# Optimization experiments

Measured on AMD Instinct MI355X. Metric: run time of the kernel, lower is better.

Reference implementation:

```python
import jax, jax.numpy as jnp
import numpy as np

N = 50000
NUM_GRAPHS = 64
EPS = 1e-16  # PyG softmax denominator epsilon


def _gat_conv(x, src, dst, W, a_src, a_dst, b, heads, out_ch):
    n = x.shape[0]
    h = (x @ W).reshape(n, heads, out_ch)                    # [N,H,C]
    al_s = jnp.einsum('nhc,hc->nh', h, a_src)                # [N,H]
    al_d = jnp.einsum('nhc,hc->nh', h, a_dst)                # [N,H]
    e = jax.nn.leaky_relu(al_s[src] + al_d[dst], 0.2)        # [E,H]
    emax = jax.ops.segment_max(e, dst, num_segments=n)       # [N,H]
    ee = jnp.exp(e - emax[dst])
    den = jax.ops.segment_sum(ee, dst, num_segments=n)       # [N,H]
    alpha = ee / (den[dst] + EPS)                            # [E,H]
    msg = h[src] * alpha[:, :, None]                         # [E,H,C]
    out = jax.ops.segment_sum(msg, dst, num_segments=n)      # [N,H,C]
    return out.reshape(n, heads * out_ch) + b


def setup_inputs() -> dict:
    key = jax.random.key(0)
    ks = jax.random.split(key, 16)
    E = 250000
    x = jax.random.normal(ks[0], (N, 11), dtype=jnp.float32)
    edge_index = jax.random.randint(ks[1], (2, E), 0, N, dtype=jnp.int64)
    batch = jnp.sort(jax.random.randint(ks[2], (N,), 0, NUM_GRAPHS, dtype=jnp.int64))
    def glorot(k, shape):
        fan = shape[0] + shape[-1]
        return jax.random.uniform(k, shape, jnp.float32, -1.0, 1.0) * np.sqrt(6.0 / fan)
    return {
        'x': x, 'edge_index': edge_index, 'batch': batch,
        'W1': glorot(ks[3], (11, 8 * 128)),
        'a1s': glorot(ks[4], (8, 128)), 'a1d': glorot(ks[5], (8, 128)),
        'b1': jnp.zeros((8 * 128,), jnp.float32),
        'W2': glorot(ks[6], (1024, 8 * 64)),
        'a2s': glorot(ks[7], (8, 64)), 'a2d': glorot(ks[8], (8, 64)),
        'b2': jnp.zeros((8 * 64,), jnp.float32),
        'W3': glorot(ks[9], (512, 4 * 32)),
        'a3s': glorot(ks[10], (4, 32)), 'a3d': glorot(ks[11], (4, 32)),
        'b3': jnp.zeros((4 * 32,), jnp.float32),
        'Wout': glorot(ks[12], (128, 1)),
        'bout': jnp.zeros((1,), jnp.float32),
    }


def reference(x, edge_index, batch, W1, a1s, a1d, b1, W2, a2s, a2d, b2,
              W3, a3s, a3d, b3, Wout, bout):
    n = x.shape[0]
    # GATConv adds self-loops by default
    loop = jnp.arange(n, dtype=edge_index.dtype)
    src = jnp.concatenate([edge_index[0], loop])
    dst = jnp.concatenate([edge_index[1], loop])
    h = jax.nn.leaky_relu(_gat_conv(x, src, dst, W1, a1s, a1d, b1, 8, 128), 0.01)
    h = jax.nn.leaky_relu(_gat_conv(h, src, dst, W2, a2s, a2d, b2, 8, 64), 0.01)
    h = jax.nn.leaky_relu(_gat_conv(h, src, dst, W3, a3s, a3d, b3, 4, 32), 0.01)
    # global mean pool over graphs
    sums = jax.ops.segment_sum(h, batch, num_segments=NUM_GRAPHS)      # [G,128]
    cnt = jax.ops.segment_sum(jnp.ones((n,), h.dtype), batch, num_segments=NUM_GRAPHS)
    pooled = sums / jnp.maximum(cnt, 1.0)[:, None]
    return pooled @ Wout + bout                                        # [G,1]
```

## Files before the change

### kernel.cpp

```cpp
#include <hip/hip_runtime.h>

#define EPS 1e-16f

typedef __attribute__((ext_vector_type(8))) short short8;
typedef __attribute__((ext_vector_type(4))) float f32x4;

__device__ __forceinline__ float b2f(unsigned short u) {
    return __uint_as_float(((unsigned)u) << 16);
}
__device__ __forceinline__ unsigned short f2b(float f) {
    unsigned u = __float_as_uint(f);
    u += 0x7fffu + ((u >> 16) & 1u);
    return (unsigned short)(u >> 16);
}

typedef __attribute__((address_space(3))) void lds_vp;
typedef __attribute__((address_space(1))) const void glb_vp;
__device__ __forceinline__ void load_lds16(const unsigned short* g,
                                           unsigned short* l) {
    __builtin_amdgcn_global_load_lds((glb_vp*)g, (lds_vp*)l, 16, 0, 0);
}

__global__ void init_deg_kernel(int* deg, int N) {
    int i = blockIdx.x * blockDim.x + threadIdx.x;
    if (i < N) deg[i] = 1;
}

__global__ void hist_kernel(const int* __restrict__ ei, int E, int N, int* deg) {
    int e = blockIdx.x * blockDim.x + threadIdx.x;
    if (e < E) {
        int d = ei[E + e];
        if ((unsigned)d < (unsigned)N) atomicAdd(&deg[d], 1);
    }
}

__global__ void scan_block_kernel(const int* __restrict__ deg,
                                  int* __restrict__ rowst,
                                  int* __restrict__ bsum, int N) {
    __shared__ int s[256];
    int t = threadIdx.x, b = blockIdx.x;
    int i = b * 256 + t;
    s[t] = (i < N) ? deg[i] : 0;
    __syncthreads();
    for (int o = 1; o < 256; o <<= 1) {
        int a = (t >= o) ? s[t - o] : 0;
        __syncthreads();
        s[t] += a;
        __syncthreads();
    }
    if (i < N) rowst[i + 1] = s[t];
    if (t == 255) bsum[b] = s[255];
}

__global__ void scan_top_kernel(const int* __restrict__ bsum,
                                int* __restrict__ boff, int NB) {
    __shared__ int psum[65];
    int t = threadIdx.x;
    int chunk = (NB + 63) / 64;
    int lo = t * chunk, hi = lo + chunk;
    if (lo > NB) lo = NB;
    if (hi > NB) hi = NB;
    int s = 0;
    for (int i = lo; i < hi; i++) s += bsum[i];
    psum[t + 1] = s;
    __syncthreads();
    if (t == 0) {
        psum[0] = 0;
        for (int i = 1; i <= 64; i++) psum[i] += psum[i - 1];
    }
    __syncthreads();
    int run = psum[t];
    for (int i = lo; i < hi; i++) {
        boff[i] = run;
        run += bsum[i];
    }
}

__global__ void scan_finish_kernel(int* __restrict__ rowst,
                                   const int* __restrict__ boff,
                                   const int* __restrict__ deg,
                                   int* __restrict__ srcs,
                                   int* __restrict__ cursor, int N) {
    int i = blockIdx.x * 256 + threadIdx.x;
    if (i == 0) rowst[0] = 0;
    if (i < N) {
        int incl = rowst[i + 1] + boff[blockIdx.x];
        rowst[i + 1] = incl;
        int st = incl - deg[i];
        srcs[st] = i;
        cursor[i] = st + 1;
    }
}

__global__ void scatter_kernel(const int* __restrict__ ei, int E, int N,
                               int* cursor, int* srcs) {
    int e = blockIdx.x * blockDim.x + threadIdx.x;
    if (e < E) {
        int d = ei[E + e];
        if ((unsigned)d < (unsigned)N) {
            int p = atomicAdd(&cursor[d], 1);
            int s = ei[e];
            if ((unsigned)s >= (unsigned)N) s = d;
            srcs[p] = s;
        }
    }
}

__global__ void wprep_kernel(const float* __restrict__ W1,
                             const float* __restrict__ W2,
                             const float* __restrict__ W3,
                             unsigned short* __restrict__ wt2,
                             unsigned short* __restrict__ wt3,
                             unsigned short* __restrict__ w1sk) {
    int i = blockIdx.x * blockDim.x + threadIdx.x;
    if (i < 1024 * 512) {
        int k = i / 512, n = i % 512;
        wt2[(size_t)n * 1024 + k] = f2b(W2[i]);
    } else if (i < 1024 * 512 + 512 * 128) {
        int j = i - 1024 * 512;
        int k = j / 128, n = j % 128;
        wt3[(size_t)n * 512 + k] = f2b(W3[j]);
    } else if (i < 1024 * 512 + 512 * 128 + 8 * 128 * 32) {
        int q = i - (1024 * 512 + 512 * 128);
        int h = q >> 12, rem = q & 4095;
        int c = rem >> 5, kk = rem & 31;
        int off = (h == 7) ? 16 : 0;
        float v = 0.f;
        int k = kk - off;
        if (k >= 0 && k < 11) v = W1[k * 1024 + h * 128 + c];
        w1sk[q] = f2b(v);
    }
}

__global__ void wa1_kernel(const float* __restrict__ W1,
                           const float* __restrict__ a1s,
                           const float* __restrict__ a1d,
                           float* __restrict__ w_as, float* __restrict__ w_ad) {
    int t = threadIdx.x;
    if (t >= 88) return;
    int h = t / 11, k = t % 11;
    float s = 0.f, d = 0.f;
    for (int c = 0; c < 128; c++) {
        float w = W1[k * 1024 + h * 128 + c];
        s += w * a1s[h * 128 + c];
        d += w * a1d[h * 128 + c];
    }
    w_as[h * 16 + k] = s;
    w_ad[h * 16 + k] = d;
}

__global__ void al1_kernel(const float* __restrict__ x,
                           const float* __restrict__ w_as,
                           const float* __restrict__ w_ad,
                           float* __restrict__ als, float* __restrict__ ald,
                           int N) {
    int i = blockIdx.x * blockDim.x + threadIdx.x;
    if (i >= N * 8) return;
    int n = i >> 3, h = i & 7;
    float s = 0.f, d = 0.f;
#pragma unroll
    for (int k = 0; k < 11; k++) {
        float xv = x[n * 11 + k];
        s += xv * w_as[h * 16 + k];
        d += xv * w_ad[h * 16 + k];
    }
    als[i] = s;
    ald[i] = d;
}

template <int H>
__global__ void mden_kernel(const float* __restrict__ als,
                            const float* __restrict__ ald,
                            const int* __restrict__ rowst,
                            const int* __restrict__ srcs,
                            float* __restrict__ escr, int N) {
    int i = blockIdx.x * blockDim.x + threadIdx.x;
    if (i >= N * H) return;
    int n = i / H, h = i % H;
    float aldn = ald[i];
    int start = rowst[n], end = rowst[n + 1];
    const int CH = 4;
    float m = -1e30f;
    for (int idx = start; idx < end; idx += CH) {
        int mc = end - idx;
        if (mc > CH) mc = CH;
        int ss[CH];
        float lv[CH];
#pragma unroll
        for (int j = 0; j < CH; j++)
            if (j < mc) ss[j] = srcs[idx + j];
#pragma unroll
        for (int j = 0; j < CH; j++)
            if (j < mc) lv[j] = als[ss[j] * H + h];
#pragma unroll
        for (int j = 0; j < CH; j++)
            if (j < mc) {
                float v = lv[j] + aldn;
                v = v > 0.f ? v : 0.2f * v;
                escr[(size_t)(idx + j) * H + h] = v;
                m = fmaxf(m, v);
            }
    }
    float den = 0.f;
    for (int idx = start; idx < end; idx += CH) {
        int mc = end - idx;
        if (mc > CH) mc = CH;
        float lv[CH];
#pragma unroll
        for (int j = 0; j < CH; j++)
            if (j < mc) lv[j] = escr[(size_t)(idx + j) * H + h];
#pragma unroll
        for (int j = 0; j < CH; j++)
            if (j < mc) den += expf(lv[j] - m);
    }
    float dinv = 1.0f / (den + EPS);
    for (int idx = start; idx < end; idx += CH) {
        int mc = end - idx;
        if (mc > CH) mc = CH;
        float lv[CH];
#pragma unroll
        for (int j = 0; j < CH; j++)
            if (j < mc) lv[j] = escr[(size_t)(idx + j) * H + h];
#pragma unroll
        for (int j = 0; j < CH; j++)
            if (j < mc)
                escr[(size_t)(idx + j) * H + h] = expf(lv[j] - m) * dinv;
    }
}

__global__ void aggx_kernel(const float* __restrict__ x,
                            const float* __restrict__ escr,
                            const int* __restrict__ rowst,
                            const int* __restrict__ srcs,
                            unsigned short* __restrict__ A2, int N) {
    int n = blockIdx.x;
    int t = threadIdx.x;
    int h = t >> 4, k = t & 15;
    int start = rowst[n], end = rowst[n + 1];
    float acc = 0.f;
    const int CH = 4;
    for (int idx = start; idx < end; idx += CH) {
        int mc = end - idx;
        if (mc > CH) mc = CH;
        int ss[CH];
        float av[CH], xv[CH];
#pragma unroll
        for (int j = 0; j < CH; j++)
            if (j < mc) ss[j] = srcs[idx + j];
#pragma unroll
        for (int j = 0; j < CH; j++)
            if (j < mc) av[j] = escr[(size_t)(idx + j) * 8 + h];
#pragma unroll
        for (int j = 0; j < CH; j++)
            if (j < mc) xv[j] = (k < 11) ? x[ss[j] * 11 + k] : 0.f;
#pragma unroll
        for (int j = 0; j < CH; j++)
            if (j < mc) acc += av[j] * xv[j];
    }
    A2[(size_t)n * 128 + t] = f2b(acc);
}

template <bool EPI, int HB, int CC, bool SK>
__global__ __launch_bounds__(256) void gemm_mfma(
    const unsigned short* __restrict__ A, const unsigned short* __restrict__ Bt,
    unsigned short* __restrict__ C, const float* __restrict__ bias,
    const float* __restrict__ a_s, const float* __restrict__ a_d,
    float* __restrict__ als, float* __restrict__ ald, int H, int M, int N,
    int K, int lda) {
    int NX = gridDim.x;
    int bid = blockIdx.y * NX + blockIdx.x;
    int win = bid & (8 * NX - 1);
    int mg = bid / (8 * NX);
    int m_t = mg * 8 + (win & 7);
    int n_t = win >> 3;
    int bm = m_t * 128, bn = n_t * 128;
    if (bm >= M) return;

    union SMem {
        struct {
            unsigned short As[2][128 * 32];
            unsigned short Bs[2][128 * 32];
        } k;
        unsigned short Ct[128 * 132];
    };
    __shared__ __align__(16) SMem sm;
    auto& As = sm.k.As;
    auto& Bs = sm.k.Bs;
    auto& Ct = sm.Ct;

    int t = threadIdx.x;
    int w = t >> 6, lane = t & 63;
    int quad = lane >> 4, l16 = lane & 15;
    int wr = (w >> 1) * 64, wc = (w & 1) * 64;

    int kofs = 0;
    const unsigned short* Bb = Bt;
    if (SK) {
        kofs = n_t * 16;
        if (kofs > lda - 32) kofs = lda - 32;
        Bb = Bt + (size_t)n_t * 128 * 32;
    }

    int c0 = w * 128 + lane;
    int c1 = c0 + 64;
    int r0 = c0 >> 2, p0 = c0 & 3;
    int r1 = c1 >> 2, p1 = c1 & 3;
    int j0 = (p0 - (r0 >> 1)) & 3;
    int j1 = (p1 - (r1 >> 1)) & 3;
    int ga0 = bm + r0;
    if (ga0 >= M) ga0 = M - 1;
    int ga1 = bm + r1;
    if (ga1 >= M) ga1 = M - 1;
    const unsigned short* Ag0 = A + (size_t)ga0 * lda + kofs + j0 * 8;
    const unsigned short* Ag1 = A + (size_t)ga1 * lda + kofs + j1 * 8;
    size_t br0 = SK ? (size_t)r0 : (size_t)(bn + r0);
    size_t br1 = SK ? (size_t)r1 : (size_t)(bn + r1);
    const unsigned short* Bg0 = Bb + br0 * K + j0 * 8;
    const unsigned short* Bg1 = Bb + br1 * K + j1 * 8;

    auto stage = [&](int st, int k0) {
        load_lds16(Ag0 + k0, &As[st][(w * 128) * 8]);
        load_lds16(Ag1 + k0, &As[st][(w * 128 + 64) * 8]);
        load_lds16(Bg0 + k0, &Bs[st][(w * 128) * 8]);
        load_lds16(Bg1 + k0, &Bs[st][(w * 128 + 64) * 8]);
    };

    int aoff[4], boff4[4];
#pragma unroll
    for (int i = 0; i < 4; i++) {
        int ra = wr + i * 16 + l16;
        aoff[i] = ra * 32 + (((quad + (ra >> 1)) & 3) * 8);
        int rb = wc + i * 16 + l16;
        boff4[i] = rb * 32 + (((quad + (rb >> 1)) & 3) * 8);
    }

    f32x4 acc[4][4] = {};
    stage(0, 0);
    int st = 0;
    for (int k0 = 0; k0 < K; k0 += 32, st ^= 1) {
        __syncthreads();
        if (k0 + 32 < K) stage(st ^ 1, k0 + 32);
        short8 a[4], b[4];
#pragma unroll
        for (int mi = 0; mi < 4; mi++) a[mi] = *(const short8*)&As[st][aoff[mi]];
#pragma unroll
        for (int ni = 0; ni < 4; ni++) b[ni] = *(const short8*)&Bs[st][boff4[ni]];
#pragma unroll
        for (int mi = 0; mi < 4; mi++)
#pragma unroll
            for (int ni = 0; ni < 4; ni++)
                acc[mi][ni] = __builtin_amdgcn_mfma_f32_16x16x32_bf16(
                    a[mi], b[ni], acc[mi][ni], 0, 0, 0);
    }
    __syncthreads();

#pragma unroll
    for (int mi = 0; mi < 4; mi++) {
#pragma unroll
        for (int r = 0; r < 4; r++) {
            int rl = wr + mi * 16 + quad * 4 + r;
#pragma unroll
            for (int ni = 0; ni < 4; ni++) {
                int cl = wc + ni * 16 + l16;
                float v = acc[mi][ni][r];
                if (EPI) {
                    v += bias[bn + cl];
                    v = v > 0.f ? v : 0.01f * v;
                }
                Ct[rl * 132 + cl] = f2b(v);
            }
        }
    }
    __syncthreads();
#pragma unroll
    for (int p = 0; p < 16; p++) {
        int q = p * 256 + t;
        int row = q >> 5, c8 = q & 31;
        if (bm + row < M) {
            uint2 v = *(const uint2*)&Ct[row * 132 + c8 * 4];
            *(uint2*)&C[(size_t)(bm + row) * N + bn + c8 * 4] = v;
        }
    }
    if (HB > 0) {
        for (int pi = t; pi < 128 * HB; pi += 256) {
            int row = pi / HB, hl = pi % HB;
            if (bm + row >= M) continue;
            int hg = bn / CC + hl;
            const unsigned short* rp = &Ct[row * 132 + hl * CC];
            const float* asp = a_s + hg * CC;
            const float* adp = a_d + hg * CC;
            float s = 0.f, d = 0.f;
#pragma unroll
            for (int c = 0; c < CC; c++) {
                float v = b2f(rp[c]);
                s += v * asp[c];
                d += v * adp[c];
            }
            als[(size_t)(bm + row) * H + hg] = s;
            ald[(size_t)(bm + row) * H + hg] = d;
        }
    }
}

template <int HB, int CC>
__global__ __launch_bounds__(256, 2) void gemm_pipe(
    const unsigned short* __restrict__ A, const unsigned short* __restrict__ Bt,
    unsigned short* __restrict__ C, const float* __restrict__ a_s,
    const float* __restrict__ a_d, float* __restrict__ als,
    float* __restrict__ ald, int H, int M, int N, int K) {
    int NX = gridDim.x;
    int bid = blockIdx.y * NX + blockIdx.x;
    int win = bid & (8 * NX - 1);
    int mg = bid / (8 * NX);
    int m_t = mg * 8 + (win & 7);
    int n_t = win >> 3;
    int bm = m_t * 128, bn = n_t * 128;
    if (bm >= M) return;

    union SMem {
        struct {
            unsigned short As[2][128 * 64];
            unsigned short Bs[2][128 * 64];
        } k;
        unsigned short Ct[128 * 132];
    };
    __shared__ __align__(16) SMem sm;

    int t = threadIdx.x;
    int w = t >> 6, lane = t & 63;
    int quad = lane >> 4, l16 = lane & 15;
    int wr = (w >> 1) * 64, wc = (w & 1) * 64;

    int srow = lane >> 3;
    int gsl = (lane & 7) ^ srow;
    const unsigned short* Ag[4];
    const unsigned short* Bg[4];
#pragma unroll
    for (int j = 0; j < 4; j++) {
        int row = (j * 4 + w) * 8 + srow;
        int ga = bm + row;
        if (ga > M - 1) ga = M - 1;
        Ag[j] = A + (size_t)ga * K + gsl * 8;
        Bg[j] = Bt + (size_t)(bn + row) * K + gsl * 8;
    }
    auto stage = [&](int st, int kt) {
        int ko = kt * 64;
#pragma unroll
        for (int j = 0; j < 4; j++) {
            load_lds16(Ag[j] + ko, &sm.k.As[st][(j * 4 + w) * 512]);
            load_lds16(Bg[j] + ko, &sm.k.Bs[st][(j * 4 + w) * 512]);
        }
    };

    int arow[4], brow[4];
#pragma unroll
    for (int i = 0; i < 4; i++) {
        arow[i] = (wr + i * 16 + l16) * 64;
        brow[i] = (wc + i * 16 + l16) * 64;
    }
    int sw = l16 & 7;

    f32x4 acc[4][4] = {};
    int NT = K >> 6;
    stage(0, 0);
    if (NT > 1) stage(1, 1);
    for (int tt = 0; tt < NT; tt++) {
        int bb = tt & 1;
        if (tt + 1 < NT)
            asm volatile("s_waitcnt vmcnt(8)" ::: "memory");
        else
            asm volatile("s_waitcnt vmcnt(0)" ::: "memory");
        __builtin_amdgcn_s_barrier();
        __builtin_amdgcn_sched_barrier(0);
#pragma unroll
        for (int ks = 0; ks < 2; ks++) {
            short8 a[4], b[4];
            int so = ((ks * 4 + quad) ^ sw) * 8;
#pragma unroll
            for (int mi = 0; mi < 4; mi++)
                a[mi] = *(const short8*)&sm.k.As[bb][arow[mi] + so];
#pragma unroll
            for (int ni = 0; ni < 4; ni++)
                b[ni] = *(const short8*)&sm.k.Bs[bb][brow[ni] + so];
            __builtin_amdgcn_s_setprio(1);
#pragma unroll
            for (int mi = 0; mi < 4; mi++)
#pragma unroll
                for (int ni = 0; ni < 4; ni++)
                    acc[mi][ni] = __builtin_amdgcn_mfma_f32_16x16x32_bf16(
                        a[mi], b[ni], acc[mi][ni], 0, 0, 0);
            __builtin_amdgcn_s_setprio(0);
        }
        asm volatile("s_waitcnt lgkmcnt(0)" ::: "memory");
        __builtin_amdgcn_s_barrier();
        if (tt + 2 < NT) stage(bb, tt + 2);
    }
    __syncthreads();

#pragma unroll
    for (int mi = 0; mi < 4; mi++) {
#pragma unroll
        for (int r = 0; r < 4; r++) {
            int rl = wr + mi * 16 + quad * 4 + r;
#pragma unroll
            for (int ni = 0; ni < 4; ni++) {
                int cl = wc + ni * 16 + l16;
                sm.Ct[rl * 132 + cl] = f2b(acc[mi][ni][r]);
            }
        }
    }
    __syncthreads();
#pragma unroll
    for (int p = 0; p < 16; p++) {
        int q = p * 256 + t;
        int row = q >> 5, c8 = q & 31;
        if (bm + row < M) {
            uint2 v = *(const uint2*)&sm.Ct[row * 132 + c8 * 4];
            *(uint2*)&C[(size_t)(bm + row) * N + bn + c8 * 4] = v;
        }
    }
    if (HB > 0) {
        for (int pi = t; pi < 128 * HB; pi += 256) {
            int row = pi / HB, hl = pi % HB;
            if (bm + row >= M) continue;
            int hg = bn / CC + hl;
            const unsigned short* rp = &sm.Ct[row * 132 + hl * CC];
            const float* asp = a_s + hg * CC;
            const float* adp = a_d + hg * CC;
            float s = 0.f, d = 0.f;
#pragma unroll
            for (int c = 0; c < CC; c++) {
                float v = b2f(rp[c]);
                s += v * asp[c];
                d += v * adp[c];
            }
            als[(size_t)(bm + row) * H + hg] = s;
            ald[(size_t)(bm + row) * H + hg] = d;
        }
    }
}

template <int H, int C>
__global__ void agg_fused4(const unsigned short* __restrict__ hin,
                           const float* __restrict__ als,
                           const float* __restrict__ ald,
                           const int* __restrict__ rowst,
                           const int* __restrict__ srcs,
                           const float* __restrict__ bias,
                           unsigned short* __restrict__ out, int N) {
    constexpr int HC = H * C;
    constexpr int NT = HC / 4;
    constexpr int TPH = C / 4;
    constexpr int MAXE = 64;
    __shared__ float sv[MAXE * H];
    __shared__ int ssrc[MAXE];
    int n = blockIdx.x;
    int t = threadIdx.x;
    int c = t * 4;
    int hh = c / C;
    int li = (c % C) / 4;
    int start = rowst[n], end = rowst[n + 1];
    int deg = end - start;
    float a0 = 0.f, a1 = 0.f, a2 = 0.f, a3 = 0.f;

    if (deg <= MAXE) {
        for (int p = t; p < deg * H; p += NT) {
            int e = p / H, h = p % H;
            int s = srcs[start + e];
            if (h == 0) ssrc[e] = s;
            float v = als[s * H + h] + ald[n * H + h];
            sv[e * H + h] = v > 0.f ? v : 0.2f * v;
        }
        __syncthreads();
        float m = -1e30f;
        for (int e = li; e < deg; e += TPH) m = fmaxf(m, sv[e * H + hh]);
#pragma unroll
        for (int o = 1; o < TPH; o <<= 1) m = fmaxf(m, __shfl_xor(m, o));
        float ee[(MAXE + TPH - 1) / TPH];
        float den = 0.f;
        {
            int k = 0;
            for (int e = li; e < deg; e += TPH, k++) {
                float x = expf(sv[e * H + hh] - m);
                ee[k] = x;
                den += x;
            }
        }
#pragma unroll
        for (int o = 1; o < TPH; o <<= 1) den += __shfl_xor(den, o);
        float dinv = 1.0f / (den + EPS);
        {
            int k = 0;
            for (int e = li; e < deg; e += TPH, k++)
                sv[e * H + hh] = ee[k] * dinv;
        }
        __syncthreads();
        const int CH = 4;
        for (int e = 0; e < deg; e += CH) {
            int mc = deg - e;
            if (mc > CH) mc = CH;
            int ss[CH];
            float al[CH];
            ushort4 uv[CH];
#pragma unroll
            for (int j = 0; j < CH; j++)
                if (j < mc) {
                    ss[j] = ssrc[e + j];
                    al[j] = sv[(e + j) * H + hh];
                }
#pragma unroll
            for (int j = 0; j < CH; j++)
                if (j < mc)
                    uv[j] = *(const ushort4*)(hin + (size_t)ss[j] * HC + c);
#pragma unroll
            for (int j = 0; j < CH; j++)
                if (j < mc) {
                    a0 += al[j] * b2f(uv[j].x);
                    a1 += al[j] * b2f(uv[j].y);
                    a2 += al[j] * b2f(uv[j].z);
                    a3 += al[j] * b2f(uv[j].w);
                }
        }
    } else {
        float aldn = ald[n * H + hh];
        float m = -1e30f;
        for (int idx = start + li; idx < end; idx += TPH) {
            float v = als[srcs[idx] * H + hh] + aldn;
            v = v > 0.f ? v : 0.2f * v;
            m = fmaxf(m, v);
        }
#pragma unroll
        for (int o = 1; o < TPH; o <<= 1) m = fmaxf(m, __shfl_xor(m, o));
        float den = 0.f;
        for (int idx = start + li; idx < end; idx += TPH) {
            float v = als[srcs[idx] * H + hh] + aldn;
            v = v > 0.f ? v : 0.2f * v;
            den += expf(v - m);
        }
#pragma unroll
        for (int o = 1; o < TPH; o <<= 1) den += __shfl_xor(den, o);
        float dinv = 1.0f / (den + EPS);
        const int CH = 4;
        for (int idx = start; idx < end; idx += CH) {
            int mc = end - idx;
            if (mc > CH) mc = CH;
            int ss[CH];
            float lv[CH];
            ushort4 uv[CH];
#pragma unroll
            for (int j = 0; j < CH; j++)
                if (j < mc) ss[j] = srcs[idx + j];
#pragma unroll
            for (int j = 0; j < CH; j++)
                if (j < mc) lv[j] = als[ss[j] * H + hh];
#pragma unroll
            for (int j = 0; j < CH; j++)
                if (j < mc)
                    uv[j] = *(const ushort4*)(hin + (size_t)ss[j] * HC + c);
#pragma unroll
            for (int j = 0; j < CH; j++)
                if (j < mc) {
                    float v = lv[j] + aldn;
                    v = v > 0.f ? v : 0.2f * v;
                    float a = expf(v - m) * dinv;
                    a0 += a * b2f(uv[j].x);
                    a1 += a * b2f(uv[j].y);
                    a2 += a * b2f(uv[j].z);
                    a3 += a * b2f(uv[j].w);
                }
        }
    }
    float v0 = a0 + bias[c], v1 = a1 + bias[c + 1];
    float v2 = a2 + bias[c + 2], v3 = a3 + bias[c + 3];
    ushort4 o;
    o.x = f2b(v0 > 0.f ? v0 : 0.01f * v0);
    o.y = f2b(v1 > 0.f ? v1 : 0.01f * v1);
    o.z = f2b(v2 > 0.f ? v2 : 0.01f * v2);
    o.w = f2b(v3 > 0.f ? v3 : 0.01f * v3);
    *(ushort4*)&out[(size_t)n * HC + c] = o;
}

template <int H, int C>
__global__ void agg_fused2(const unsigned short* __restrict__ hin,
                           const float* __restrict__ als,
                           const float* __restrict__ ald,
                           const int* __restrict__ rowst,
                           const int* __restrict__ srcs,
                           const float* __restrict__ bias,
                           unsigned short* __restrict__ out, int N) {
    constexpr int HC = H * C;
    constexpr int NT = HC / 2;
    constexpr int TPH = C / 2;
    constexpr int MAXE = 64;
    __shared__ float sv[MAXE * H];
    __shared__ int ssrc[MAXE];
    int n = blockIdx.x;
    int t = threadIdx.x;
    int c = t * 2;
    int hh = c / C;
    int li = (c % C) / 2;
    int start = rowst[n], end = rowst[n + 1];
    int deg = end - start;
    float a0 = 0.f, a1 = 0.f;

    if (deg <= MAXE) {
        for (int p = t; p < deg * H; p += NT) {
            int e = p / H, h = p % H;
            int s = srcs[start + e];
            if (h == 0) ssrc[e] = s;
            float v = als[s * H + h] + ald[n * H + h];
            sv[e * H + h] = v > 0.f ? v : 0.2f * v;
        }
        __syncthreads();
        float m = -1e30f;
        for (int e = li; e < deg; e += TPH) m = fmaxf(m, sv[e * H + hh]);
#pragma unroll
        for (int o = 1; o < TPH; o <<= 1) m = fmaxf(m, __shfl_xor(m, o));
        float ee[(MAXE + TPH - 1) / TPH];
        float den = 0.f;
        {
            int k = 0;
            for (int e = li; e < deg; e += TPH, k++) {
                float x = expf(sv[e * H + hh] - m);
                ee[k] = x;
                den += x;
            }
        }
#pragma unroll
        for (int o = 1; o < TPH; o <<= 1) den += __shfl_xor(den, o);
        float dinv = 1.0f / (den + EPS);
        {
            int k = 0;
            for (int e = li; e < deg; e += TPH, k++)
                sv[e * H + hh] = ee[k] * dinv;
        }
        __syncthreads();
        const int CH = 4;
        for (int e = 0; e < deg; e += CH) {
            int mc = deg - e;
            if (mc > CH) mc = CH;
            int ss[CH];
            float al[CH];
            ushort2 uv[CH];
#pragma unroll
            for (int j = 0; j < CH; j++)
                if (j < mc) {
                    ss[j] = ssrc[e + j];
                    al[j] = sv[(e + j) * H + hh];
                }
#pragma unroll
            for (int j = 0; j < CH; j++)
                if (j < mc)
                    uv[j] = *(const ushort2*)(hin + (size_t)ss[j] * HC + c);
#pragma unroll
            for (int j = 0; j < CH; j++)
                if (j < mc) {
                    a0 += al[j] * b2f(uv[j].x);
                    a1 += al[j] * b2f(uv[j].y);
                }
        }
    } else {
        float aldn = ald[n * H + hh];
        float m = -1e30f;
        for (int idx = start + li; idx < end; idx += TPH) {
            float v = als[srcs[idx] * H + hh] + aldn;
            v = v > 0.f ? v : 0.2f * v;
            m = fmaxf(m, v);
        }
#pragma unroll
        for (int o = 1; o < TPH; o <<= 1) m = fmaxf(m, __shfl_xor(m, o));
        float den = 0.f;
        for (int idx = start + li; idx < end; idx += TPH) {
            float v = als[srcs[idx] * H + hh] + aldn;
            v = v > 0.f ? v : 0.2f * v;
            den += expf(v - m);
        }
#pragma unroll
        for (int o = 1; o < TPH; o <<= 1) den += __shfl_xor(den, o);
        float dinv = 1.0f / (den + EPS);
        const int CH = 4;
        for (int idx = start; idx < end; idx += CH) {
            int mc = end - idx;
            if (mc > CH) mc = CH;
            int ss[CH];
            float lv[CH];
            ushort2 uv[CH];
#pragma unroll
            for (int j = 0; j < CH; j++)
                if (j < mc) ss[j] = srcs[idx + j];
#pragma unroll
            for (int j = 0; j < CH; j++)
                if (j < mc) lv[j] = als[ss[j] * H + hh];
#pragma unroll
            for (int j = 0; j < CH; j++)
                if (j < mc)
                    uv[j] = *(const ushort2*)(hin + (size_t)ss[j] * HC + c);
#pragma unroll
            for (int j = 0; j < CH; j++)
                if (j < mc) {
                    float v = lv[j] + aldn;
                    v = v > 0.f ? v : 0.2f * v;
                    float a = expf(v - m) * dinv;
                    a0 += a * b2f(uv[j].x);
                    a1 += a * b2f(uv[j].y);
                }
        }
    }
    float v0 = a0 + bias[c], v1 = a1 + bias[c + 1];
    ushort2 o;
    o.x = f2b(v0 > 0.f ? v0 : 0.01f * v0);
    o.y = f2b(v1 > 0.f ? v1 : 0.01f * v1);
    *(ushort2*)&out[(size_t)n * HC + c] = o;
}

__global__ void pool_init_kernel(float* pool, int GC) {
    int i = blockIdx.x * blockDim.x + threadIdx.x;
    if (i < GC) pool[i] = 0.f;
}

__global__ void pool_partial_kernel(const unsigned short* __restrict__ h3,
                                    const int* __restrict__ batch,
                                    float* __restrict__ pool, int N, int G) {
    int lo = blockIdx.x * 128;
    int hi = lo + 128;
    if (hi > N) hi = N;
    if (lo >= N) return;
    int t = threadIdx.x;
    int cur = batch[lo];
    float acc = 0.f;
    for (int n = lo; n < hi; n++) {
        int g = batch[n];
        if (g != cur) {
            if ((unsigned)cur < (unsigned)G) atomicAdd(&pool[cur * 128 + t], acc);
            acc = 0.f;
            cur = g;
        }
        acc += b2f(h3[(size_t)n * 128 + t]);
    }
    if ((unsigned)cur < (unsigned)G) atomicAdd(&pool[cur * 128 + t], acc);
}

__global__ void head_kernel(const float* __restrict__ pool,
                            const int* __restrict__ batch,
                            const float* __restrict__ Wout,
                            const float* __restrict__ bout,
                            float* __restrict__ out, int N) {
    int g = blockIdx.x;
    int t = threadIdx.x;
    int lo, hi;
    {
        int a = 0, b = N;
        while (a < b) { int mid = (a + b) >> 1; if (batch[mid] < g) a = mid + 1; else b = mid; }
        lo = a;
        a = lo; b = N;
        while (a < b) { int mid = (a + b) >> 1; if (batch[mid] < g + 1) a = mid + 1; else b = mid; }
        hi = a;
    }
    float c = (float)(hi - lo);
    c = c > 1.f ? c : 1.f;
    float v = (pool[g * 128 + t] / c) * Wout[t];
    for (int o = 32; o; o >>= 1) v += __shfl_xor(v, o);
    __shared__ float partial[2];
    if ((t & 63) == 0) partial[t >> 6] = v;
    __syncthreads();
    if (t == 0) out[g] = partial[0] + partial[1] + bout[0];
}

extern "C" void kernel_launch(void* const* d_in, const int* in_sizes, int n_in,
                              void* d_out, int out_size, void* d_ws,
                              size_t ws_size, hipStream_t stream) {
    const float* x = (const float*)d_in[0];
    const int* ei = (const int*)d_in[1];
    const int* batch = (const int*)d_in[2];
    const float* W1 = (const float*)d_in[3];
    const float* a1s = (const float*)d_in[4];
    const float* a1d = (const float*)d_in[5];
    const float* b1 = (const float*)d_in[6];
    const float* W2 = (const float*)d_in[7];
    const float* a2s = (const float*)d_in[8];
    const float* a2d = (const float*)d_in[9];
    const float* b2 = (const float*)d_in[10];
    const float* W3 = (const float*)d_in[11];
    const float* a3s = (const float*)d_in[12];
    const float* a3d = (const float*)d_in[13];
    const float* b3 = (const float*)d_in[14];
    const float* Wout = (const float*)d_in[15];
    const float* bout = (const float*)d_in[16];
    float* out = (float*)d_out;

    const int N = in_sizes[0] / 11;
    const int E = in_sizes[1] / 2;
    const int Etot = E + N;
    const int G = out_size;
    const int NB = (N + 255) / 256;
    const int MT = ((N + 127) / 128 + 7) / 8 * 8;

    char* ws = (char*)d_ws;
    size_t off = 0;
    auto alloc = [&](size_t bytes) -> void* {
        void* p = ws + off;
        off += (bytes + 255) & ~(size_t)255;
        return p;
    };
    unsigned short* buf1 = (unsigned short*)alloc((size_t)N * 1024 * 2);
    unsigned short* buf2 = (unsigned short*)alloc((size_t)N * 1024 * 2);
    float* als = (float*)alloc((size_t)N * 8 * 4);
    float* ald = (float*)alloc((size_t)N * 8 * 4);
    float* escr = (float*)alloc((size_t)Etot * 8 * 4);
    int* rowst = (int*)alloc((size_t)(N + 1) * 4);
    int* cursor = (int*)alloc((size_t)N * 4);
    int* srcs = (int*)alloc((size_t)Etot * 4);
    int* deg = (int*)alloc((size_t)N * 4);
    int* bsum = (int*)alloc((size_t)NB * 4);
    int* boff = (int*)alloc((size_t)NB * 4);
    float* pool = (float*)alloc((size_t)G * 128 * 4);
    unsigned short* aggx = (unsigned short*)alloc((size_t)N * 128 * 2);
    unsigned short* w1sk = (unsigned short*)alloc((size_t)8 * 128 * 32 * 2);
    unsigned short* wt2 = (unsigned short*)alloc((size_t)1024 * 512 * 2);
    unsigned short* wt3 = (unsigned short*)alloc((size_t)512 * 128 * 2);
    float* w_as = (float*)alloc(8 * 16 * 4);
    float* w_ad = (float*)alloc(8 * 16 * 4);

    int nb = (N + 255) / 256;
    int eb = (E + 255) / 256;

    init_deg_kernel<<<nb, 256, 0, stream>>>(deg, N);
    hist_kernel<<<eb, 256, 0, stream>>>(ei, E, N, deg);
    scan_block_kernel<<<NB, 256, 0, stream>>>(deg, rowst, bsum, N);
    scan_top_kernel<<<1, 64, 0, stream>>>(bsum, boff, NB);
    scan_finish_kernel<<<NB, 256, 0, stream>>>(rowst, boff, deg, srcs, cursor,
                                               N);
    scatter_kernel<<<eb, 256, 0, stream>>>(ei, E, N, cursor, srcs);

    const int WTOT = 1024 * 512 + 512 * 128 + 8 * 128 * 32;
    wprep_kernel<<<(WTOT + 255) / 256, 256, 0, stream>>>(W1, W2, W3, wt2, wt3,
                                                         w1sk);
    wa1_kernel<<<1, 128, 0, stream>>>(W1, a1s, a1d, w_as, w_ad);

    al1_kernel<<<(N * 8 + 255) / 256, 256, 0, stream>>>(x, w_as, w_ad, als, ald,
                                                        N);
    mden_kernel<8><<<(N * 8 + 255) / 256, 256, 0, stream>>>(als, ald, rowst,
                                                            srcs, escr, N);
    aggx_kernel<<<N, 128, 0, stream>>>(x, escr, rowst, srcs, aggx, N);
    gemm_mfma<true, 0, 1, true><<<dim3(8, MT), 256, 0, stream>>>(
        aggx, w1sk, buf2, b1, nullptr, nullptr, nullptr, nullptr, 0, N, 1024,
        32, 128);

    gemm_pipe<2, 64><<<dim3(4, MT), 256, 0, stream>>>(
        buf2, wt2, buf1, a2s, a2d, als, ald, 8, N, 512, 1024);
    agg_fused4<8, 64><<<N, 128, 0, stream>>>(buf1, als, ald, rowst, srcs, b2,
                                             buf2, N);

    gemm_pipe<4, 32><<<dim3(1, MT), 256, 0, stream>>>(
        buf2, wt3, buf1, a3s, a3d, als, ald, 4, N, 128, 512);
    agg_fused2<4, 32><<<N, 64, 0, stream>>>(buf1, als, ald, rowst, srcs, b3,
                                            buf2, N);

    pool_init_kernel<<<(G * 128 + 255) / 256, 256, 0, stream>>>(pool, G * 128);
    pool_partial_kernel<<<(N + 127) / 128, 128, 0, stream>>>(buf2, batch, pool,
                                                             N, G);
    head_kernel<<<G, 128, 0, stream>>>(pool, batch, Wout, bout, out, N);
}
```

Measured before the change: 453.3 us.

## Use 256x256 tile GEMM with XCD-aware block swizzle for layer-2 projection

Replaces the 128x128-tile pipelined GEMM for the second GAT layer (N x 1024 -> 512) with a new kernel using 256x256 tiles, 8x8 MFMA accumulators per wave, double-buffered direct-to-LDS loads and an XCD-aware block remapping. The larger tile raises arithmetic intensity and reduces redundant A/B reads from global memory, while the fused attention-logit epilogue is kept and done in two 128-row halves through LDS. The cost is heavy register pressure (256 accumulators per lane, occupancy 1), fewer workgroups (about 392) for 256 CUs, and 128KB of LDS staging.

```diff
diff --git a/kernel.cpp b/kernel.cpp
--- a/kernel.cpp
+++ b/kernel.cpp
@@ -402,6 +402,152 @@
     }
 }
 
+__global__ __launch_bounds__(256, 1) void gemm_big(
+    const unsigned short* __restrict__ A, const unsigned short* __restrict__ Bt,
+    unsigned short* __restrict__ C, const float* __restrict__ a_s,
+    const float* __restrict__ a_d, float* __restrict__ als,
+    float* __restrict__ ald, int H, int M, int N, int K) {
+    int nnt = N >> 8;
+    int nwg = gridDim.x;
+    int bid = blockIdx.x;
+    int q = nwg >> 3, r = nwg & 7;
+    int xcd = bid & 7, idx = bid >> 3;
+    int base = (xcd < r) ? xcd * (q + 1) : r * (q + 1) + (xcd - r) * q;
+    int swz = base + idx;
+    int m_t = swz / nnt, n_t = swz % nnt;
+    int bm = m_t * 256, bn = n_t * 256;
+    if (bm >= M) return;
+
+    union SMem {
+        struct {
+            unsigned short Ah[2][256 * 64];
+            unsigned short Bh[2][256 * 64];
+        } k;
+        unsigned short Ct[128 * 264];
+    };
+    __shared__ __align__(16) SMem sm;
+
+    int t = threadIdx.x;
+    int w = t >> 6, lane = t & 63;
+    int quad = lane >> 4, l16 = lane & 15;
+    int wr = (w >> 1) * 128, wc = (w & 1) * 128;
+
+    int csrow = (w * 64 + lane) >> 3;
+    int gs = (lane & 7) ^ (csrow & 7);
+    const unsigned short* Ag[8];
+    const unsigned short* Bg[8];
+#pragma unroll
+    for (int rnd = 0; rnd < 8; rnd++) {
+        int rowA = bm + csrow + rnd * 32;
+        if (rowA > M - 1) rowA = M - 1;
+        Ag[rnd] = A + (size_t)rowA * K + gs * 8;
+        Bg[rnd] = Bt + (size_t)(bn + csrow + rnd * 32) * K + gs * 8;
+    }
+    auto stage = [&](int st, int kt) {
+        int ko = kt * 64;
+#pragma unroll
+        for (int rnd = 0; rnd < 8; rnd++) {
+            load_lds16(Ag[rnd] + ko, &sm.k.Ah[st][(rnd * 256 + w * 64) * 8]);
+            load_lds16(Bg[rnd] + ko, &sm.k.Bh[st][(rnd * 256 + w * 64) * 8]);
+        }
+    };
+
+    int arow[8], browf[8];
+#pragma unroll
+    for (int i = 0; i < 8; i++) {
+        arow[i] = (wr + i * 16 + l16) * 64;
+        browf[i] = (wc + i * 16 + l16) * 64;
+    }
+    int sw = l16 & 7;
+
+    f32x4 acc[8][8] = {};
+    int NT = K >> 6;
+    stage(0, 0);
+    stage(1, 1);
+    for (int tt = 0; tt < NT; tt++) {
+        int db = tt & 1;
+        if (tt + 1 < NT)
+            asm volatile("s_waitcnt vmcnt(16)" ::: "memory");
+        else
+            asm volatile("s_waitcnt vmcnt(0)" ::: "memory");
+        __builtin_amdgcn_s_barrier();
+        __builtin_amdgcn_sched_barrier(0);
+#pragma unroll 1
+        for (int ks = 0; ks < 2; ks++) {
+            short8 a[8], b[8];
+            int so = ((ks * 4 + quad) ^ sw) * 8;
+#pragma unroll
+            for (int mi = 0; mi < 8; mi++)
+                a[mi] = *(const short8*)&sm.k.Ah[db][arow[mi] + so];
+#pragma unroll
+            for (int ni = 0; ni < 8; ni++)
+                b[ni] = *(const short8*)&sm.k.Bh[db][browf[ni] + so];
+            __builtin_amdgcn_s_setprio(1);
+#pragma unroll
+            for (int mi = 0; mi < 8; mi++)
+#pragma unroll
+                for (int ni = 0; ni < 8; ni++)
+                    acc[mi][ni] = __builtin_amdgcn_mfma_f32_16x16x32_bf16(
+                        a[mi], b[ni], acc[mi][ni], 0, 0, 0);
+            __builtin_amdgcn_s_setprio(0);
+        }
+        asm volatile("s_waitcnt lgkmcnt(0)" ::: "memory");
+        __builtin_amdgcn_s_barrier();
+        if (tt + 2 < NT) stage(db, tt + 2);
+    }
+    __syncthreads();
+
+    for (int h = 0; h < 2; h++) {
+        if ((w >> 1) == h) {
+#pragma unroll
+            for (int mi = 0; mi < 8; mi++) {
+#pragma unroll
+                for (int rr = 0; rr < 4; rr++) {
+                    int rl = mi * 16 + quad * 4 + rr;
+#pragma unroll
+                    for (int ni = 0; ni < 8; ni++) {
+                        int cl = wc + ni * 16 + l16;
+                        sm.Ct[rl * 264 + cl] = f2b(acc[mi][ni][rr]);
+                    }
+                }
+            }
+        }
+        __syncthreads();
+#pragma unroll
+        for (int p = 0; p < 16; p++) {
+            int qq = p * 256 + t;
+            int row = qq >> 5, c8 = qq & 31;
+            int gr = bm + h * 128 + row;
+            if (gr < M) {
+                uint4 v = *(const uint4*)&sm.Ct[row * 264 + c8 * 8];
+                *(uint4*)&C[(size_t)gr * N + bn + c8 * 8] = v;
+            }
+        }
+#pragma unroll
+        for (int pp = 0; pp < 2; pp++) {
+            int pi = pp * 256 + t;
+            int row = pi >> 2, hl = pi & 3;
+            int gr = bm + h * 128 + row;
+            if (gr < M) {
+                int hg = (bn >> 6) + hl;
+                const unsigned short* rp = &sm.Ct[row * 264 + hl * 64];
+                const float* asp = a_s + hg * 64;
+                const float* adp = a_d + hg * 64;
+                float s = 0.f, d = 0.f;
+#pragma unroll
+                for (int c = 0; c < 64; c++) {
+                    float v = b2f(rp[c]);
+                    s += v * asp[c];
+                    d += v * adp[c];
+                }
+                als[(size_t)gr * H + hg] = s;
+                ald[(size_t)gr * H + hg] = d;
+            }
+        }
+        __syncthreads();
+    }
+}
+
 template <int HB, int CC>
 __global__ __launch_bounds__(256, 2) void gemm_pipe(
     const unsigned short* __restrict__ A, const unsigned short* __restrict__ Bt,
@@ -894,6 +1040,7 @@
     const int G = out_size;
     const int NB = (N + 255) / 256;
     const int MT = ((N + 127) / 128 + 7) / 8 * 8;
+    const int MT256 = (N + 255) / 256;
 
     char* ws = (char*)d_ws;
     size_t off = 0;
@@ -946,8 +1093,8 @@
         aggx, w1sk, buf2, b1, nullptr, nullptr, nullptr, nullptr, 0, N, 1024,
         32, 128);
 
-    gemm_pipe<2, 64><<<dim3(4, MT), 256, 0, stream>>>(
-        buf2, wt2, buf1, a2s, a2d, als, ald, 8, N, 512, 1024);
+    gemm_big<<<MT256 * 2, 256, 0, stream>>>(buf2, wt2, buf1, a2s, a2d, als,
+                                            ald, 8, N, 512, 1024);
     agg_fused4<8, 64><<<N, 128, 0, stream>>>(buf1, als, ald, rowst, srcs, b2,
                                              buf2, N);
 
```

Result: slower. 475.6 us (+4.9%).
